# Kernel tuning notes

Hardware: AMD Instinct MI355X
Metric: run time of the kernel (lower is better)

Reference implementation:

```python
import jax, jax.numpy as jnp
import numpy as np

B, C, H, W_DIM = 32, 512, 56, 56
C_INTER = C // 2
EPS = 1e-5


def _conv1x1(x, w, b):
    # 1x1 conv == per-pixel matmul over channels. w: [out, in], b: [out]
    return jnp.einsum('bchw,oc->bohw', x, w) + b[None, :, None, None]


def setup_inputs() -> dict:
    key = jax.random.key(0)
    ks = jax.random.split(key, 5)
    s_in = 1.0 / np.sqrt(C)
    s_mid = 1.0 / np.sqrt(C_INTER)
    return {
        'x': jax.random.normal(ks[0], (B, C, H, W_DIM), dtype=jnp.float32),
        'g_w': jax.random.normal(ks[1], (C_INTER, C), dtype=jnp.float32) * s_in,
        'g_b': jnp.zeros((C_INTER,), dtype=jnp.float32),
        'theta_w': jax.random.normal(ks[2], (C_INTER, C), dtype=jnp.float32) * s_in,
        'theta_b': jnp.zeros((C_INTER,), dtype=jnp.float32),
        'phi_w': jax.random.normal(ks[3], (C_INTER, C), dtype=jnp.float32) * s_in,
        'phi_b': jnp.zeros((C_INTER,), dtype=jnp.float32),
        'W_w': jax.random.normal(ks[4], (C, C_INTER), dtype=jnp.float32) * s_mid,
        'W_b': jnp.zeros((C,), dtype=jnp.float32),
        'gamma': jnp.ones((C,), dtype=jnp.float32),
        'beta': jnp.zeros((C,), dtype=jnp.float32),
    }


def reference(x, g_w, g_b, theta_w, theta_b, phi_w, phi_b, W_w, W_b, gamma, beta):
    b, c, h, w = x.shape
    n = h * w
    g_x = _conv1x1(x, g_w, g_b).reshape(b, C_INTER, n)        # [B, C', N]
    theta_x = _conv1x1(x, theta_w, theta_b).reshape(b, C_INTER, n)
    phi_x = _conv1x1(x, phi_w, phi_b).reshape(b, C_INTER, n)
    # f = theta @ phi^T / N : small [B, C', C'] channel Gram matrix
    f_div_C = jnp.einsum('bcn,bdn->bcd', theta_x, phi_x) / n
    y = jnp.einsum('bcd,bdn->bcn', f_div_C, g_x).reshape(b, C_INTER, h, w)
    z = _conv1x1(y, W_w, W_b) + x
    # BatchNorm2d (training mode): normalize with batch stats over (B,H,W)
    mean = jnp.mean(z, axis=(0, 2, 3), keepdims=True)
    var = jnp.var(z, axis=(0, 2, 3), keepdims=True)
    z_hat = (z - mean) * jax.lax.rsqrt(var + EPS)
    return z_hat * gamma[None, :, None, None] + beta[None, :, None, None]
```

## Files before the change

kernel.cpp:

```cpp
#include <hip/hip_runtime.h>

#define Bn   32
#define Cc   512
#define CIc  256
#define Nsp  3136
#define Npad 3200
#define EPSbn 1e-5f

typedef __attribute__((ext_vector_type(8))) short v8s;
typedef __attribute__((ext_vector_type(4))) float v4f;

__device__ __forceinline__ unsigned short f2bf(float f) {
    unsigned int u = __builtin_bit_cast(unsigned int, f);
    u += 0x7fffu + ((u >> 16) & 1u);
    return (unsigned short)(u >> 16);
}

__device__ __forceinline__ float bf2f(unsigned short u) {
    unsigned int x = ((unsigned int)u) << 16;
    return __builtin_bit_cast(float, x);
}

__device__ __forceinline__ void async16(const unsigned short* g, unsigned short* l) {
    __builtin_amdgcn_global_load_lds(
        (const __attribute__((address_space(1))) unsigned int*)g,
        (__attribute__((address_space(3))) unsigned int*)l, 16, 0, 0);
}

template <int EPI>
__global__ __launch_bounds__(256)
void mfma_gemm(const unsigned short* __restrict__ A, int lda, long a_bs,
               const unsigned short* __restrict__ B, int ldb, long b_bs,
               void* __restrict__ Out, int ldo, long o_bs,
               int K, float scale,
               const float* __restrict__ biasN, long bN_bs,
               const float* __restrict__ xres,
               float* __restrict__ stats,
               const float* __restrict__ r2u1, const float* __restrict__ r2w1,
               const float* __restrict__ r2u2, const float* __restrict__ r2w2)
{
    __shared__ __align__(16) unsigned short As[128 * 32];
    __shared__ __align__(16) unsigned short Bs[128 * 32];

    const int tid  = threadIdx.x;
    const int w    = tid >> 6;
    const int lane = tid & 63;
    const int b    = blockIdx.z;
    const int m0   = blockIdx.x * 128;
    const int n0   = blockIdx.y * 128;

    const unsigned short* Ab = A + (long)b * a_bs;
    const unsigned short* Bb = B + (long)b * b_bs;

    const int ldrow = 32 * w + (lane >> 2);
    const int ldk   = (lane & 3) * 8;
    unsigned short* lA0 = &As[(2 * w + 0) * 512];
    unsigned short* lA1 = &As[(2 * w + 1) * 512];
    unsigned short* lB0 = &Bs[(2 * w + 0) * 512];
    unsigned short* lB1 = &Bs[(2 * w + 1) * 512];
    const size_t aoff0 = (size_t)(m0 + ldrow) * lda + ldk;
    const size_t aoff1 = aoff0 + (size_t)16 * lda;
    const size_t boff0 = (size_t)(n0 + ldrow) * ldb + ldk;
    const size_t boff1 = boff0 + (size_t)16 * ldb;

    const int wm = (w & 1) * 64;
    const int wn = (w >> 1) * 64;
    const int fr = lane & 15;
    const int fk = (lane >> 4) * 8;

    v4f acc[4][4] = {};

    for (int k0 = 0; k0 < K; k0 += 32) {
        __syncthreads();
        async16(Ab + aoff0 + k0, lA0);
        async16(Ab + aoff1 + k0, lA1);
        async16(Bb + boff0 + k0, lB0);
        async16(Bb + boff1 + k0, lB1);
        __syncthreads();

        v8s af[4], bf[4];
#pragma unroll
        for (int i = 0; i < 4; ++i)
            af[i] = *(const v8s*)&As[(wm + i * 16 + fr) * 32 + fk];
#pragma unroll
        for (int j = 0; j < 4; ++j)
            bf[j] = *(const v8s*)&Bs[(wn + j * 16 + fr) * 32 + fk];
#pragma unroll
        for (int i = 0; i < 4; ++i)
#pragma unroll
            for (int j = 0; j < 4; ++j)
                acc[i][j] = __builtin_amdgcn_mfma_f32_16x16x32_bf16(af[i], bf[j], acc[i][j], 0, 0, 0);
    }

    const int em = wm + ((lane >> 4) << 2);
    const int en = wn + fr;

    if constexpr (EPI == 0) {
        unsigned short* O = (unsigned short*)Out;
#pragma unroll
        for (int j = 0; j < 4; ++j) {
            const int gn = n0 + en + j * 16;
            const float bN = biasN ? biasN[bN_bs * b + gn] : 0.0f;
            unsigned short* orow = O + (long)b * o_bs + (size_t)gn * ldo + m0 + em;
#pragma unroll
            for (int i = 0; i < 4; ++i) {
                ushort4 o4;
                o4.x = f2bf(acc[i][j].x * scale + bN);
                o4.y = f2bf(acc[i][j].y * scale + bN);
                o4.z = f2bf(acc[i][j].z * scale + bN);
                o4.w = f2bf(acc[i][j].w * scale + bN);
                *(ushort4*)&orow[i * 16] = o4;
            }
        }
    } else if constexpr (EPI == 4) {
        unsigned short* O = (unsigned short*)Out;
#pragma unroll
        for (int j = 0; j < 4; ++j) {
            const int gn = n0 + en + j * 16;
            const float uu1 = r2u1[(size_t)b * Cc + gn];
            const float uu2 = r2u2[gn];
            unsigned short* orow = O + (long)b * o_bs + (size_t)gn * ldo + m0 + em;
#pragma unroll
            for (int i = 0; i < 4; ++i) {
                const int e0 = m0 + em + i * 16;
                const float4 w1v = *(const float4*)&r2w1[e0];
                const float4 w2v = *(const float4*)&r2w2[(size_t)b * Cc + e0];
                ushort4 o4;
                o4.x = f2bf(acc[i][j].x * scale + uu1 * w1v.x + uu2 * w2v.x);
                o4.y = f2bf(acc[i][j].y * scale + uu1 * w1v.y + uu2 * w2v.y);
                o4.z = f2bf(acc[i][j].z * scale + uu1 * w1v.z + uu2 * w2v.z);
                o4.w = f2bf(acc[i][j].w * scale + uu1 * w1v.w + uu2 * w2v.w);
                *(ushort4*)&orow[i * 16] = o4;
            }
        }
    } else {
        unsigned short* O = (unsigned short*)Out;
        float sj[4] = {0.f, 0.f, 0.f, 0.f}, qj[4] = {0.f, 0.f, 0.f, 0.f};
#pragma unroll
        for (int j = 0; j < 4; ++j) {
            const int gc = n0 + en + j * 16;
            const float wb = biasN[bN_bs * b + gc];
            const float* xrow = xres + (size_t)b * Cc * Nsp + (size_t)gc * Nsp;
            unsigned short* zrow = O + (long)b * o_bs + (size_t)gc * ldo;
#pragma unroll
            for (int i = 0; i < 4; ++i) {
                const int gsp = m0 + em + i * 16;
                if (gsp < Nsp) {
                    const float4 xr = *(const float4*)&xrow[gsp];
                    const float z0 = acc[i][j].x + wb + xr.x;
                    const float z1 = acc[i][j].y + wb + xr.y;
                    const float z2 = acc[i][j].z + wb + xr.z;
                    const float z3 = acc[i][j].w + wb + xr.w;
                    sj[j] += z0 + z1 + z2 + z3;
                    qj[j] += z0 * z0 + z1 * z1 + z2 * z2 + z3 * z3;
                    ushort4 o4;
                    o4.x = f2bf(z0); o4.y = f2bf(z1); o4.z = f2bf(z2); o4.w = f2bf(z3);
                    *(ushort4*)&zrow[gsp] = o4;
                }
            }
        }
        __syncthreads();
        float* red = (float*)As;
        const int cid = (lane >> 4) + ((w & 1) << 2);
#pragma unroll
        for (int j = 0; j < 4; ++j) {
            const int cc = wn + fr + j * 16;
            red[cc * 8 + cid] = sj[j];
            red[1024 + cc * 8 + cid] = qj[j];
        }
        __syncthreads();
        if (tid < 128) {
            float s = 0.f, q = 0.f;
#pragma unroll
            for (int t = 0; t < 8; ++t) { s += red[tid * 8 + t]; q += red[1024 + tid * 8 + t]; }
            atomicAdd(&stats[n0 + tid], s);
            atomicAdd(&stats[Cc + n0 + tid], q);
        }
    }
}

__global__ __launch_bounds__(256)
void cast_transpose(const float* __restrict__ x, unsigned short* __restrict__ xT,
                    unsigned short* __restrict__ x16, float* __restrict__ r)
{
    __shared__ float tile[64][65];
    const int b  = blockIdx.z;
    const int n0 = blockIdx.x * 64;
    const int c0 = blockIdx.y * 64;
    const float* xb = x + (size_t)b * Cc * Nsp;
    unsigned short* x16b = x16 + (size_t)b * Cc * Nsp;
    const int t = threadIdx.x;
    const int tr  = t >> 4;
    const int tc4 = (t & 15) * 4;
#pragma unroll
    for (int i = 0; i < 4; ++i) {
        const int c = tr + i * 16;
        const float4 v = *(const float4*)&xb[(size_t)(c0 + c) * Nsp + n0 + tc4];
        tile[tc4 + 0][c] = v.x;
        tile[tc4 + 1][c] = v.y;
        tile[tc4 + 2][c] = v.z;
        tile[tc4 + 3][c] = v.w;
        ushort4 s;
        s.x = f2bf(v.x); s.y = f2bf(v.y); s.z = f2bf(v.z); s.w = f2bf(v.w);
        *(ushort4*)&x16b[(size_t)(c0 + c) * Nsp + n0 + tc4] = s;
    }
    __syncthreads();
    if (t < 64) {
        float s = 0.f;
#pragma unroll 8
        for (int n = 0; n < 64; ++n) s += tile[n][t];
        atomicAdd(&r[(size_t)b * Cc + c0 + t], s);
    }
    unsigned short* xo = xT + (size_t)b * Nsp * Cc;
#pragma unroll
    for (int i = 0; i < 4; ++i) {
        const int n = tr + i * 16;
        ushort4 o;
        o.x = f2bf(tile[n][tc4 + 0]);
        o.y = f2bf(tile[n][tc4 + 1]);
        o.z = f2bf(tile[n][tc4 + 2]);
        o.w = f2bf(tile[n][tc4 + 3]);
        *(ushort4*)&xo[(size_t)(n0 + n) * Cc + c0 + tc4] = o;
    }
}

__global__ void cast_w(const float* __restrict__ src, unsigned short* __restrict__ dst, int n)
{
    const int i = (blockIdx.x * 256 + threadIdx.x) * 4;
    if (i < n) {
        const float4 v = *(const float4*)&src[i];
        ushort4 o;
        o.x = f2bf(v.x); o.y = f2bf(v.y); o.z = f2bf(v.z); o.w = f2bf(v.w);
        *(ushort4*)&dst[i] = o;
    }
}

__global__ void cast_wT(const float* __restrict__ src, unsigned short* __restrict__ dst)
{
    const int c = blockIdx.x;
    const int d = threadIdx.x;
    dst[(size_t)c * CIc + d] = f2bf(src[(size_t)d * Cc + c]);
}

__global__ void k_vec1(const float* __restrict__ g_w, const float* __restrict__ ph_w,
                       const float* __restrict__ W_w, const float* __restrict__ th_b,
                       const float* __restrict__ ph_b, const float* __restrict__ g_b,
                       float* __restrict__ w1, float* __restrict__ q,
                       float* __restrict__ u2, float* __restrict__ pbgb)
{
    const int t = threadIdx.x;
    float a = 0.f, bq = 0.f;
    for (int d = 0; d < CIc; ++d) {
        a  += g_w[(size_t)d * Cc + t] * ph_b[d];
        bq += ph_w[(size_t)d * Cc + t] * g_b[d];
    }
    w1[t] = a; q[t] = bq;
    float u = 0.f;
    for (int c = 0; c < CIc; ++c) u += W_w[(size_t)t * CIc + c] * th_b[c];
    u2[t] = u;
    if (t == 0) {
        float s = 0.f;
        for (int d = 0; d < CIc; ++d) s += ph_b[d] * g_b[d];
        *pbgb = s;
    }
}

__global__ void k_vecb(const unsigned short* __restrict__ S, const unsigned short* __restrict__ WT,
                       const unsigned short* __restrict__ PGt, const float* __restrict__ r,
                       const float* __restrict__ w1, const float* __restrict__ q,
                       const float* __restrict__ pbgb,
                       const float* __restrict__ th_w, const float* __restrict__ th_b,
                       const float* __restrict__ W_w, const float* __restrict__ W_b,
                       float* __restrict__ u1, float* __restrict__ w2, float* __restrict__ c0)
{
    const int b = blockIdx.x, t = threadIdx.x;
    __shared__ float sq[Cc];
    __shared__ float fgb[CIc];
    __shared__ float s_rq;
    const float invN = 1.0f / (float)Nsp;
    const float* rb = r + (size_t)b * Cc;

    float aq = 0.f;
    const unsigned short* Sr = S + (size_t)b * Cc * Cc + (size_t)t * Cc;
    for (int c2 = 0; c2 < Cc; ++c2) aq += bf2f(Sr[c2]) * q[c2];
    sq[t] = aq;

    float a1 = 0.f;
    const unsigned short* WTr = WT + (size_t)t * Cc;
    for (int c1 = 0; c1 < Cc; ++c1) a1 += bf2f(WTr[c1]) * rb[c1];
    u1[(size_t)b * Cc + t] = a1 * invN;

    float a2 = 0.f;
    const unsigned short* PGr = PGt + (size_t)t * Cc;
    for (int c2 = 0; c2 < Cc; ++c2) a2 += bf2f(PGr[c2]) * rb[c2];
    w2[(size_t)b * Cc + t] = a2 * invN + w1[t];

    if (t == 0) {
        float s = 0.f;
        for (int c2 = 0; c2 < Cc; ++c2) s += rb[c2] * q[c2];
        s_rq = s;
    }
    __syncthreads();
    if (t < CIc) {
        float ts = 0.f, tr2 = 0.f;
        const float* thr = th_w + (size_t)t * Cc;
        for (int c1 = 0; c1 < Cc; ++c1) { ts += thr[c1] * sq[c1]; tr2 += thr[c1] * rb[c1]; }
        const float pg = *pbgb;
        fgb[t] = (ts + pg * tr2 + s_rq * th_b[t]) * invN + pg * th_b[t];
    }
    __syncthreads();
    float cacc = 0.f;
    const float* Wr = W_w + (size_t)t * CIc;
    for (int d = 0; d < CIc; ++d) cacc += Wr[d] * fgb[d];
    c0[(size_t)b * Cc + t] = cacc + W_b[t];
}

__global__ void finalize_stats(const float* __restrict__ stats, float* __restrict__ mstd)
{
    const int c = threadIdx.x;
    const float inv = 1.0f / (float)((long)Bn * Nsp);
    const float mean = stats[c] * inv;
    const float var  = stats[Cc + c] * inv - mean * mean;
    mstd[c] = mean;
    mstd[Cc + c] = rsqrtf(var + EPSbn);
}

__global__ __launch_bounds__(256)
void bnorm_apply(const unsigned short* __restrict__ z, const float* __restrict__ mstd,
                 const float* __restrict__ gamma, const float* __restrict__ beta,
                 float* __restrict__ out)
{
    const int NG = Bn * Cc * (Nsp / 8);
    const int g = blockIdx.x * 256 + threadIdx.x;
    if (g >= NG) return;
    const int c = (g / (Nsp / 8)) & (Cc - 1);
    const float a1 = mstd[Cc + c] * gamma[c];
    const float a0 = beta[c] - mstd[c] * a1;
    const v8s zv = *(const v8s*)(z + (size_t)g * 8);
    float* op = out + (size_t)g * 8;
    float4 o0, o1;
    o0.x = bf2f((unsigned short)zv[0]) * a1 + a0;
    o0.y = bf2f((unsigned short)zv[1]) * a1 + a0;
    o0.z = bf2f((unsigned short)zv[2]) * a1 + a0;
    o0.w = bf2f((unsigned short)zv[3]) * a1 + a0;
    o1.x = bf2f((unsigned short)zv[4]) * a1 + a0;
    o1.y = bf2f((unsigned short)zv[5]) * a1 + a0;
    o1.z = bf2f((unsigned short)zv[6]) * a1 + a0;
    o1.w = bf2f((unsigned short)zv[7]) * a1 + a0;
    *(float4*)op = o0;
    *(float4*)(op + 4) = o1;
}

extern "C" void kernel_launch(void* const* d_in, const int* in_sizes, int n_in,
                              void* d_out, int out_size, void* d_ws, size_t ws_size,
                              hipStream_t stream)
{
    const float* x     = (const float*)d_in[0];
    const float* g_w   = (const float*)d_in[1];
    const float* g_b   = (const float*)d_in[2];
    const float* th_w  = (const float*)d_in[3];
    const float* th_b  = (const float*)d_in[4];
    const float* ph_w  = (const float*)d_in[5];
    const float* ph_b  = (const float*)d_in[6];
    const float* W_w   = (const float*)d_in[7];
    const float* W_b   = (const float*)d_in[8];
    const float* gamma = (const float*)d_in[9];
    const float* beta  = (const float*)d_in[10];
    float* out = (float*)d_out;

    unsigned short* xT   = (unsigned short*)d_ws;
    unsigned short* x16  = xT + (size_t)Bn * Nsp * Cc + 64 * Cc;
    unsigned short* S    = x16 + (size_t)Bn * Cc * Nsp;
    unsigned short* WT   = S + (size_t)Bn * Cc * Cc;
    unsigned short* PGt  = WT + (size_t)Cc * Cc;
    unsigned short* thwT = PGt + (size_t)Cc * Cc;
    unsigned short* phwT = thwT + (size_t)Cc * CIc;
    unsigned short* gwT  = phwT + (size_t)Cc * CIc;
    unsigned short* Ww16 = gwT + (size_t)Cc * CIc;
    float* r    = (float*)(Ww16 + (size_t)Cc * CIc);
    float* w1   = r + Bn * Cc;
    float* q    = w1 + Cc;
    float* u2v  = q + Cc;
    float* pbgb = u2v + Cc;
    float* u1v  = pbgb + 4;
    float* w2v  = u1v + Bn * Cc;
    float* c0   = w2v + Bn * Cc;
    float* stats = c0 + Bn * Cc;
    float* mstd  = stats + 2 * Cc;

    unsigned short* Rt    = x16;
    unsigned short* Afull = S;
    unsigned short* z16   = x16;

    hipMemsetAsync(stats, 0, 2 * Cc * sizeof(float), stream);
    hipMemsetAsync(r, 0, (size_t)Bn * Cc * sizeof(float), stream);

    const dim3 blk(256);
    const long xT_bs  = (long)Nsp * Cc;
    const long x16_bs = (long)Cc * Nsp;
    const long sq_bs  = (long)Cc * Cc;

    cast_transpose<<<dim3(49, 8, Bn), blk, 0, stream>>>(x, xT, x16, r);
    cast_w<<<dim3(128), blk, 0, stream>>>(W_w, Ww16, Cc * CIc);
    cast_wT<<<dim3(Cc), dim3(CIc), 0, stream>>>(th_w, thwT);
    cast_wT<<<dim3(Cc), dim3(CIc), 0, stream>>>(ph_w, phwT);
    cast_wT<<<dim3(Cc), dim3(CIc), 0, stream>>>(g_w, gwT);
    k_vec1<<<dim3(1), dim3(Cc), 0, stream>>>(g_w, ph_w, W_w, th_b, ph_b, g_b, w1, q, u2v, pbgb);

    mfma_gemm<0><<<dim3(4, 4, 1), blk, 0, stream>>>(
        thwT, CIc, 0, Ww16, CIc, 0, WT, Cc, 0, CIc, 1.0f,
        nullptr, 0, nullptr, nullptr, nullptr, nullptr, nullptr, nullptr);
    mfma_gemm<0><<<dim3(4, 4, 1), blk, 0, stream>>>(
        phwT, CIc, 0, gwT, CIc, 0, PGt, Cc, 0, CIc, 1.0f,
        nullptr, 0, nullptr, nullptr, nullptr, nullptr, nullptr, nullptr);
    mfma_gemm<0><<<dim3(4, 4, Bn), blk, 0, stream>>>(
        x16, Nsp, x16_bs, x16, Nsp, x16_bs, S, Cc, sq_bs, Nsp, 1.0f,
        nullptr, 0, nullptr, nullptr, nullptr, nullptr, nullptr, nullptr);
    mfma_gemm<0><<<dim3(4, 4, Bn), blk, 0, stream>>>(
        S, Cc, sq_bs, PGt, Cc, 0, Rt, Cc, sq_bs, Cc, 1.0f,
        nullptr, 0, nullptr, nullptr, nullptr, nullptr, nullptr, nullptr);
    k_vecb<<<dim3(Bn), dim3(Cc), 0, stream>>>(S, WT, PGt, r, w1, q, pbgb,
                                              th_w, th_b, W_w, W_b, u1v, w2v, c0);
    mfma_gemm<4><<<dim3(4, 4, Bn), blk, 0, stream>>>(
        Rt, Cc, sq_bs, WT, Cc, 0, Afull, Cc, sq_bs, Cc, 1.0f / (float)Nsp,
        nullptr, 0, nullptr, nullptr, u1v, w1, u2v, w2v);
    mfma_gemm<2><<<dim3(25, 4, Bn), blk, 0, stream>>>(
        xT, Cc, xT_bs, Afull, Cc, sq_bs, z16, Nsp, (long)Cc * Nsp, Cc, 1.0f,
        c0, Cc, x, stats, nullptr, nullptr, nullptr, nullptr);
    finalize_stats<<<dim3(1), dim3(Cc), 0, stream>>>(stats, mstd);
    bnorm_apply<<<dim3((Bn * Cc * (Nsp / 8) + 255) / 256), blk, 0, stream>>>(
        z16, mstd, gamma, beta, out);
}
```

Baseline: 866.1 us.

## Compute BatchNorm stats analytically from Gram matrices and fuse normalize into final GEMM

BatchNorm batch statistics are now derived algebraically from the per-batch Gram matrix S, the fused operator Afull, and per-channel row sums and sums of squares of x, using an extra small GEMM (S·Afull) and a reduction kernel. This removes the bf16 z intermediate and the separate normalize pass, because the final large GEMM can apply scale and shift directly and write fp32 output. The final GEMM also loops over all four N chunks inside one block so the xT tile is reused. In exchange it adds a 512x512 batched GEMM and more workspace, and the statistics rely on bf16-rounded operands, which may cost accuracy.

```diff
diff --git a/kernel.cpp b/kernel.cpp
--- a/kernel.cpp
+++ b/kernel.cpp
@@ -4,7 +4,6 @@
 #define Cc   512
 #define CIc  256
 #define Nsp  3136
-#define Npad 3200
 #define EPSbn 1e-5f
 
 typedef __attribute__((ext_vector_type(8))) short v8s;
@@ -27,15 +26,15 @@
         (__attribute__((address_space(3))) unsigned int*)l, 16, 0, 0);
 }
 
-template <int EPI>
+template <int EPI, int NCH>
 __global__ __launch_bounds__(256)
 void mfma_gemm(const unsigned short* __restrict__ A, int lda, long a_bs,
                const unsigned short* __restrict__ B, int ldb, long b_bs,
                void* __restrict__ Out, int ldo, long o_bs,
                int K, float scale,
                const float* __restrict__ biasN, long bN_bs,
-               const float* __restrict__ xres,
-               float* __restrict__ stats,
+               const void* __restrict__ xres,
+               const float* __restrict__ a10,
                const float* __restrict__ r2u1, const float* __restrict__ r2w1,
                const float* __restrict__ r2u2, const float* __restrict__ r2w2)
 {
@@ -47,7 +46,6 @@
     const int lane = tid & 63;
     const int b    = blockIdx.z;
     const int m0   = blockIdx.x * 128;
-    const int n0   = blockIdx.y * 128;
 
     const unsigned short* Ab = A + (long)b * a_bs;
     const unsigned short* Bb = B + (long)b * b_bs;
@@ -60,128 +58,115 @@
     unsigned short* lB1 = &Bs[(2 * w + 1) * 512];
     const size_t aoff0 = (size_t)(m0 + ldrow) * lda + ldk;
     const size_t aoff1 = aoff0 + (size_t)16 * lda;
-    const size_t boff0 = (size_t)(n0 + ldrow) * ldb + ldk;
-    const size_t boff1 = boff0 + (size_t)16 * ldb;
 
     const int wm = (w & 1) * 64;
     const int wn = (w >> 1) * 64;
     const int fr = lane & 15;
     const int fk = (lane >> 4) * 8;
 
-    v4f acc[4][4] = {};
-
-    for (int k0 = 0; k0 < K; k0 += 32) {
-        __syncthreads();
-        async16(Ab + aoff0 + k0, lA0);
-        async16(Ab + aoff1 + k0, lA1);
-        async16(Bb + boff0 + k0, lB0);
-        async16(Bb + boff1 + k0, lB1);
-        __syncthreads();
-
-        v8s af[4], bf[4];
-#pragma unroll
-        for (int i = 0; i < 4; ++i)
-            af[i] = *(const v8s*)&As[(wm + i * 16 + fr) * 32 + fk];
-#pragma unroll
-        for (int j = 0; j < 4; ++j)
-            bf[j] = *(const v8s*)&Bs[(wn + j * 16 + fr) * 32 + fk];
-#pragma unroll
-        for (int i = 0; i < 4; ++i)
-#pragma unroll
-            for (int j = 0; j < 4; ++j)
-                acc[i][j] = __builtin_amdgcn_mfma_f32_16x16x32_bf16(af[i], bf[j], acc[i][j], 0, 0, 0);
-    }
-
     const int em = wm + ((lane >> 4) << 2);
     const int en = wn + fr;
 
-    if constexpr (EPI == 0) {
-        unsigned short* O = (unsigned short*)Out;
-#pragma unroll
-        for (int j = 0; j < 4; ++j) {
-            const int gn = n0 + en + j * 16;
-            const float bN = biasN ? biasN[bN_bs * b + gn] : 0.0f;
-            unsigned short* orow = O + (long)b * o_bs + (size_t)gn * ldo + m0 + em;
-#pragma unroll
-            for (int i = 0; i < 4; ++i) {
-                ushort4 o4;
-                o4.x = f2bf(acc[i][j].x * scale + bN);
-                o4.y = f2bf(acc[i][j].y * scale + bN);
-                o4.z = f2bf(acc[i][j].z * scale + bN);
-                o4.w = f2bf(acc[i][j].w * scale + bN);
-                *(ushort4*)&orow[i * 16] = o4;
+    for (int nc = 0; nc < NCH; ++nc) {
+        const int n0 = (NCH == 1 ? (int)blockIdx.y : nc) * 128;
+        const size_t boff0 = (size_t)(n0 + ldrow) * ldb + ldk;
+        const size_t boff1 = boff0 + (size_t)16 * ldb;
+
+        v4f acc[4][4] = {};
+
+        for (int k0 = 0; k0 < K; k0 += 32) {
+            __syncthreads();
+            async16(Ab + aoff0 + k0, lA0);
+            async16(Ab + aoff1 + k0, lA1);
+            async16(Bb + boff0 + k0, lB0);
+            async16(Bb + boff1 + k0, lB1);
+            __syncthreads();
+
+            v8s af[4], bf[4];
+#pragma unroll
+            for (int i = 0; i < 4; ++i)
+                af[i] = *(const v8s*)&As[(wm + i * 16 + fr) * 32 + fk];
+#pragma unroll
+            for (int j = 0; j < 4; ++j)
+                bf[j] = *(const v8s*)&Bs[(wn + j * 16 + fr) * 32 + fk];
+#pragma unroll
+            for (int i = 0; i < 4; ++i)
+#pragma unroll
+                for (int j = 0; j < 4; ++j)
+                    acc[i][j] = __builtin_amdgcn_mfma_f32_16x16x32_bf16(af[i], bf[j], acc[i][j], 0, 0, 0);
+        }
+
+        if constexpr (EPI == 0) {
+            unsigned short* O = (unsigned short*)Out;
+#pragma unroll
+            for (int j = 0; j < 4; ++j) {
+                const int gn = n0 + en + j * 16;
+                const float bN = biasN ? biasN[bN_bs * b + gn] : 0.0f;
+                unsigned short* orow = O + (long)b * o_bs + (size_t)gn * ldo + m0 + em;
+#pragma unroll
+                for (int i = 0; i < 4; ++i) {
+                    ushort4 o4;
+                    o4.x = f2bf(acc[i][j].x * scale + bN);
+                    o4.y = f2bf(acc[i][j].y * scale + bN);
+                    o4.z = f2bf(acc[i][j].z * scale + bN);
+                    o4.w = f2bf(acc[i][j].w * scale + bN);
+                    *(ushort4*)&orow[i * 16] = o4;
+                }
             }
-        }
-    } else if constexpr (EPI == 4) {
-        unsigned short* O = (unsigned short*)Out;
-#pragma unroll
-        for (int j = 0; j < 4; ++j) {
-            const int gn = n0 + en + j * 16;
-            const float uu1 = r2u1[(size_t)b * Cc + gn];
-            const float uu2 = r2u2[gn];
-            unsigned short* orow = O + (long)b * o_bs + (size_t)gn * ldo + m0 + em;
-#pragma unroll
-            for (int i = 0; i < 4; ++i) {
-                const int e0 = m0 + em + i * 16;
-                const float4 w1v = *(const float4*)&r2w1[e0];
-                const float4 w2v = *(const float4*)&r2w2[(size_t)b * Cc + e0];
-                ushort4 o4;
-                o4.x = f2bf(acc[i][j].x * scale + uu1 * w1v.x + uu2 * w2v.x);
-                o4.y = f2bf(acc[i][j].y * scale + uu1 * w1v.y + uu2 * w2v.y);
-                o4.z = f2bf(acc[i][j].z * scale + uu1 * w1v.z + uu2 * w2v.z);
-                o4.w = f2bf(acc[i][j].w * scale + uu1 * w1v.w + uu2 * w2v.w);
-                *(ushort4*)&orow[i * 16] = o4;
+        } else if constexpr (EPI == 4) {
+            unsigned short* O = (unsigned short*)Out;
+#pragma unroll
+            for (int j = 0; j < 4; ++j) {
+                const int gn = n0 + en + j * 16;
+                const float uu1 = r2u1[(size_t)b * Cc + gn];
+                const float uu2 = r2u2[gn];
+                unsigned short* orow = O + (long)b * o_bs + (size_t)gn * ldo + m0 + em;
+#pragma unroll
+                for (int i = 0; i < 4; ++i) {
+                    const int e0 = m0 + em + i * 16;
+                    const float4 w1v = *(const float4*)&r2w1[e0];
+                    const float4 w2v = *(const float4*)&r2w2[(size_t)b * Cc + e0];
+                    ushort4 o4;
+                    o4.x = f2bf(acc[i][j].x * scale + uu1 * w1v.x + uu2 * w2v.x);
+                    o4.y = f2bf(acc[i][j].y * scale + uu1 * w1v.y + uu2 * w2v.y);
+                    o4.z = f2bf(acc[i][j].z * scale + uu1 * w1v.z + uu2 * w2v.z);
+                    o4.w = f2bf(acc[i][j].w * scale + uu1 * w1v.w + uu2 * w2v.w);
+                    *(ushort4*)&orow[i * 16] = o4;
+                }
             }
-        }
-    } else {
-        unsigned short* O = (unsigned short*)Out;
-        float sj[4] = {0.f, 0.f, 0.f, 0.f}, qj[4] = {0.f, 0.f, 0.f, 0.f};
-#pragma unroll
-        for (int j = 0; j < 4; ++j) {
-            const int gc = n0 + en + j * 16;
-            const float wb = biasN[bN_bs * b + gc];
-            const float* xrow = xres + (size_t)b * Cc * Nsp + (size_t)gc * Nsp;
-            unsigned short* zrow = O + (long)b * o_bs + (size_t)gc * ldo;
-#pragma unroll
-            for (int i = 0; i < 4; ++i) {
-                const int gsp = m0 + em + i * 16;
-                if (gsp < Nsp) {
-                    const float4 xr = *(const float4*)&xrow[gsp];
-                    const float z0 = acc[i][j].x + wb + xr.x;
-                    const float z1 = acc[i][j].y + wb + xr.y;
-                    const float z2 = acc[i][j].z + wb + xr.z;
-                    const float z3 = acc[i][j].w + wb + xr.w;
-                    sj[j] += z0 + z1 + z2 + z3;
-                    qj[j] += z0 * z0 + z1 * z1 + z2 * z2 + z3 * z3;
-                    ushort4 o4;
-                    o4.x = f2bf(z0); o4.y = f2bf(z1); o4.z = f2bf(z2); o4.w = f2bf(z3);
-                    *(ushort4*)&zrow[gsp] = o4;
+        } else {
+            float* O = (float*)Out;
+            const unsigned short* xr16 = (const unsigned short*)xres;
+#pragma unroll
+            for (int j = 0; j < 4; ++j) {
+                const int gc = n0 + en + j * 16;
+                const float a1 = a10[gc];
+                const float a0 = a10[Cc + gc];
+                const float cc0 = biasN[bN_bs * b + gc];
+                const unsigned short* xrow = xr16 + (size_t)b * Cc * Nsp + (size_t)gc * Nsp;
+                float* orow = O + (long)b * o_bs + (size_t)gc * (size_t)ldo;
+#pragma unroll
+                for (int i = 0; i < 4; ++i) {
+                    const int gsp = m0 + em + i * 16;
+                    if (gsp < Nsp) {
+                        const ushort4 xr = *(const ushort4*)&xrow[gsp];
+                        float4 o;
+                        o.x = (acc[i][j].x + cc0 + bf2f(xr.x)) * a1 + a0;
+                        o.y = (acc[i][j].y + cc0 + bf2f(xr.y)) * a1 + a0;
+                        o.z = (acc[i][j].z + cc0 + bf2f(xr.z)) * a1 + a0;
+                        o.w = (acc[i][j].w + cc0 + bf2f(xr.w)) * a1 + a0;
+                        *(float4*)&orow[gsp] = o;
+                    }
                 }
             }
         }
-        __syncthreads();
-        float* red = (float*)As;
-        const int cid = (lane >> 4) + ((w & 1) << 2);
-#pragma unroll
-        for (int j = 0; j < 4; ++j) {
-            const int cc = wn + fr + j * 16;
-            red[cc * 8 + cid] = sj[j];
-            red[1024 + cc * 8 + cid] = qj[j];
-        }
-        __syncthreads();
-        if (tid < 128) {
-            float s = 0.f, q = 0.f;
-#pragma unroll
-            for (int t = 0; t < 8; ++t) { s += red[tid * 8 + t]; q += red[1024 + tid * 8 + t]; }
-            atomicAdd(&stats[n0 + tid], s);
-            atomicAdd(&stats[Cc + n0 + tid], q);
-        }
     }
 }
 
 __global__ __launch_bounds__(256)
 void cast_transpose(const float* __restrict__ x, unsigned short* __restrict__ xT,
-                    unsigned short* __restrict__ x16, float* __restrict__ r)
+                    unsigned short* __restrict__ x16, float* __restrict__ r,
+                    float* __restrict__ p)
 {
     __shared__ float tile[64][65];
     const int b  = blockIdx.z;
@@ -192,6 +177,7 @@
     const int t = threadIdx.x;
     const int tr  = t >> 4;
     const int tc4 = (t & 15) * 4;
+    float rs[4], ps[4];
 #pragma unroll
     for (int i = 0; i < 4; ++i) {
         const int c = tr + i * 16;
@@ -203,14 +189,26 @@
         ushort4 s;
         s.x = f2bf(v.x); s.y = f2bf(v.y); s.z = f2bf(v.z); s.w = f2bf(v.w);
         *(ushort4*)&x16b[(size_t)(c0 + c) * Nsp + n0 + tc4] = s;
+        const float b0 = bf2f(s.x), b1 = bf2f(s.y), b2 = bf2f(s.z), b3 = bf2f(s.w);
+        rs[i] = b0 + b1 + b2 + b3;
+        ps[i] = b0 * b0 + b1 * b1 + b2 * b2 + b3 * b3;
+    }
+#pragma unroll
+    for (int i = 0; i < 4; ++i) {
+#pragma unroll
+        for (int off = 8; off; off >>= 1) {
+            rs[i] += __shfl_down(rs[i], off, 16);
+            ps[i] += __shfl_down(ps[i], off, 16);
+        }
+    }
+    if ((t & 15) == 0) {
+#pragma unroll
+        for (int i = 0; i < 4; ++i) {
+            atomicAdd(&r[(size_t)b * Cc + c0 + tr + i * 16], rs[i]);
+            atomicAdd(&p[(size_t)b * Cc + c0 + tr + i * 16], ps[i]);
+        }
     }
     __syncthreads();
-    if (t < 64) {
-        float s = 0.f;
-#pragma unroll 8
-        for (int n = 0; n < 64; ++n) s += tile[n][t];
-        atomicAdd(&r[(size_t)b * Cc + c0 + t], s);
-    }
     unsigned short* xo = xT + (size_t)b * Nsp * Cc;
 #pragma unroll
     for (int i = 0; i < 4; ++i) {
@@ -315,40 +313,54 @@
     c0[(size_t)b * Cc + t] = cacc + W_b[t];
 }
 
-__global__ void finalize_stats(const float* __restrict__ stats, float* __restrict__ mstd)
+__global__ __launch_bounds__(256)
+void k_stats(const unsigned short* __restrict__ Afull, const unsigned short* __restrict__ AS,
+             const float* __restrict__ r, const float* __restrict__ p,
+             const float* __restrict__ c0, float* __restrict__ stats)
+{
+    const int b = blockIdx.x;
+    const int f = blockIdx.y * 4 + (threadIdx.x >> 6);
+    const int lane = threadIdx.x & 63;
+    const size_t row = ((size_t)b * Cc + f) * Cc;
+    const v8s av = *(const v8s*)(Afull + row + lane * 8);
+    const v8s sv = *(const v8s*)(AS + row + lane * 8);
+    const float* rb = r + (size_t)b * Cc + lane * 8;
+    float d1 = 0.f, ar = 0.f;
+#pragma unroll
+    for (int k = 0; k < 8; ++k) {
+        const float a = bf2f((unsigned short)av[k]);
+        d1 += a * bf2f((unsigned short)sv[k]);
+        ar += a * rb[k];
+    }
+#pragma unroll
+    for (int off = 32; off; off >>= 1) {
+        d1 += __shfl_down(d1, off);
+        ar += __shfl_down(ar, off);
+    }
+    if (lane == 0) {
+        const float cc   = c0[(size_t)b * Cc + f];
+        const float rf   = r[(size_t)b * Cc + f];
+        const float pf   = p[(size_t)b * Cc + f];
+        const float asff = bf2f(AS[row + f]);
+        const float sum = ar + rf + (float)Nsp * cc;
+        const float ss  = d1 + 2.f * cc * ar + (float)Nsp * cc * cc
+                        + 2.f * asff + 2.f * cc * rf + pf;
+        atomicAdd(&stats[f], sum);
+        atomicAdd(&stats[Cc + f], ss);
+    }
+}
+
+__global__ void finalize_stats(const float* __restrict__ stats,
+                               const float* __restrict__ gamma, const float* __restrict__ beta,
+                               float* __restrict__ a10)
 {
     const int c = threadIdx.x;
     const float inv = 1.0f / (float)((long)Bn * Nsp);
     const float mean = stats[c] * inv;
     const float var  = stats[Cc + c] * inv - mean * mean;
-    mstd[c] = mean;
-    mstd[Cc + c] = rsqrtf(var + EPSbn);
-}
-
-__global__ __launch_bounds__(256)
-void bnorm_apply(const unsigned short* __restrict__ z, const float* __restrict__ mstd,
-                 const float* __restrict__ gamma, const float* __restrict__ beta,
-                 float* __restrict__ out)
-{
-    const int NG = Bn * Cc * (Nsp / 8);
-    const int g = blockIdx.x * 256 + threadIdx.x;
-    if (g >= NG) return;
-    const int c = (g / (Nsp / 8)) & (Cc - 1);
-    const float a1 = mstd[Cc + c] * gamma[c];
-    const float a0 = beta[c] - mstd[c] * a1;
-    const v8s zv = *(const v8s*)(z + (size_t)g * 8);
-    float* op = out + (size_t)g * 8;
-    float4 o0, o1;
-    o0.x = bf2f((unsigned short)zv[0]) * a1 + a0;
-    o0.y = bf2f((unsigned short)zv[1]) * a1 + a0;
-    o0.z = bf2f((unsigned short)zv[2]) * a1 + a0;
-    o0.w = bf2f((unsigned short)zv[3]) * a1 + a0;
-    o1.x = bf2f((unsigned short)zv[4]) * a1 + a0;
-    o1.y = bf2f((unsigned short)zv[5]) * a1 + a0;
-    o1.z = bf2f((unsigned short)zv[6]) * a1 + a0;
-    o1.w = bf2f((unsigned short)zv[7]) * a1 + a0;
-    *(float4*)op = o0;
-    *(float4*)(op + 4) = o1;
+    const float a1 = rsqrtf(var + EPSbn) * gamma[c];
+    a10[c] = a1;
+    a10[Cc + c] = beta[c] - mean * a1;
 }
 
 extern "C" void kernel_launch(void* const* d_in, const int* in_sizes, int n_in,
@@ -371,14 +383,17 @@
     unsigned short* xT   = (unsigned short*)d_ws;
     unsigned short* x16  = xT + (size_t)Bn * Nsp * Cc + 64 * Cc;
     unsigned short* S    = x16 + (size_t)Bn * Cc * Nsp;
-    unsigned short* WT   = S + (size_t)Bn * Cc * Cc;
+    unsigned short* R1   = S + (size_t)Bn * Cc * Cc;
+    unsigned short* R2   = R1 + (size_t)Bn * Cc * Cc;
+    unsigned short* WT   = R2 + (size_t)Bn * Cc * Cc;
     unsigned short* PGt  = WT + (size_t)Cc * Cc;
     unsigned short* thwT = PGt + (size_t)Cc * Cc;
     unsigned short* phwT = thwT + (size_t)Cc * CIc;
     unsigned short* gwT  = phwT + (size_t)Cc * CIc;
     unsigned short* Ww16 = gwT + (size_t)Cc * CIc;
     float* r    = (float*)(Ww16 + (size_t)Cc * CIc);
-    float* w1   = r + Bn * Cc;
+    float* p    = r + Bn * Cc;
+    float* w1   = p + Bn * Cc;
     float* q    = w1 + Cc;
     float* u2v  = q + Cc;
     float* pbgb = u2v + Cc;
@@ -386,48 +401,50 @@
     float* w2v  = u1v + Bn * Cc;
     float* c0   = w2v + Bn * Cc;
     float* stats = c0 + Bn * Cc;
-    float* mstd  = stats + 2 * Cc;
-
-    unsigned short* Rt    = x16;
-    unsigned short* Afull = S;
-    unsigned short* z16   = x16;
+    float* a10   = stats + 2 * Cc;
+
+    unsigned short* Rt    = R1;
+    unsigned short* Afull = R2;
+    unsigned short* AS    = R1;
 
     hipMemsetAsync(stats, 0, 2 * Cc * sizeof(float), stream);
-    hipMemsetAsync(r, 0, (size_t)Bn * Cc * sizeof(float), stream);
+    hipMemsetAsync(r, 0, 2 * (size_t)Bn * Cc * sizeof(float), stream);
 
     const dim3 blk(256);
     const long xT_bs  = (long)Nsp * Cc;
     const long x16_bs = (long)Cc * Nsp;
     const long sq_bs  = (long)Cc * Cc;
 
-    cast_transpose<<<dim3(49, 8, Bn), blk, 0, stream>>>(x, xT, x16, r);
+    cast_transpose<<<dim3(49, 8, Bn), blk, 0, stream>>>(x, xT, x16, r, p);
     cast_w<<<dim3(128), blk, 0, stream>>>(W_w, Ww16, Cc * CIc);
     cast_wT<<<dim3(Cc), dim3(CIc), 0, stream>>>(th_w, thwT);
     cast_wT<<<dim3(Cc), dim3(CIc), 0, stream>>>(ph_w, phwT);
     cast_wT<<<dim3(Cc), dim3(CIc), 0, stream>>>(g_w, gwT);
     k_vec1<<<dim3(1), dim3(Cc), 0, stream>>>(g_w, ph_w, W_w, th_b, ph_b, g_b, w1, q, u2v, pbgb);
 
-    mfma_gemm<0><<<dim3(4, 4, 1), blk, 0, stream>>>(
+    mfma_gemm<0, 1><<<dim3(4, 4, 1), blk, 0, stream>>>(
         thwT, CIc, 0, Ww16, CIc, 0, WT, Cc, 0, CIc, 1.0f,
         nullptr, 0, nullptr, nullptr, nullptr, nullptr, nullptr, nullptr);
-    mfma_gemm<0><<<dim3(4, 4, 1), blk, 0, stream>>>(
+    mfma_gemm<0, 1><<<dim3(4, 4, 1), blk, 0, stream>>>(
         phwT, CIc, 0, gwT, CIc, 0, PGt, Cc, 0, CIc, 1.0f,
         nullptr, 0, nullptr, nullptr, nullptr, nullptr, nullptr, nullptr);
-    mfma_gemm<0><<<dim3(4, 4, Bn), blk, 0, stream>>>(
+    mfma_gemm<0, 1><<<dim3(4, 4, Bn), blk, 0, stream>>>(
         x16, Nsp, x16_bs, x16, Nsp, x16_bs, S, Cc, sq_bs, Nsp, 1.0f,
         nullptr, 0, nullptr, nullptr, nullptr, nullptr, nullptr, nullptr);
-    mfma_gemm<0><<<dim3(4, 4, Bn), blk, 0, stream>>>(
+    mfma_gemm<0, 1><<<dim3(4, 4, Bn), blk, 0, stream>>>(
         S, Cc, sq_bs, PGt, Cc, 0, Rt, Cc, sq_bs, Cc, 1.0f,
         nullptr, 0, nullptr, nullptr, nullptr, nullptr, nullptr, nullptr);
     k_vecb<<<dim3(Bn), dim3(Cc), 0, stream>>>(S, WT, PGt, r, w1, q, pbgb,
                                               th_w, th_b, W_w, W_b, u1v, w2v, c0);
-    mfma_gemm<4><<<dim3(4, 4, Bn), blk, 0, stream>>>(
+    mfma_gemm<4, 1><<<dim3(4, 4, Bn), blk, 0, stream>>>(
         Rt, Cc, sq_bs, WT, Cc, 0, Afull, Cc, sq_bs, Cc, 1.0f / (float)Nsp,
         nullptr, 0, nullptr, nullptr, u1v, w1, u2v, w2v);
-    mfma_gemm<2><<<dim3(25, 4, Bn), blk, 0, stream>>>(
-        xT, Cc, xT_bs, Afull, Cc, sq_bs, z16, Nsp, (long)Cc * Nsp, Cc, 1.0f,
-        c0, Cc, x, stats, nullptr, nullptr, nullptr, nullptr);
-    finalize_stats<<<dim3(1), dim3(Cc), 0, stream>>>(stats, mstd);
-    bnorm_apply<<<dim3((Bn * Cc * (Nsp / 8) + 255) / 256), blk, 0, stream>>>(
-        z16, mstd, gamma, beta, out);
-}
+    mfma_gemm<0, 1><<<dim3(4, 4, Bn), blk, 0, stream>>>(
+        S, Cc, sq_bs, Afull, Cc, sq_bs, AS, Cc, sq_bs, Cc, 1.0f,
+        nullptr, 0, nullptr, nullptr, nullptr, nullptr, nullptr, nullptr);
+    k_stats<<<dim3(Bn, 128), blk, 0, stream>>>(Afull, AS, r, p, c0, stats);
+    finalize_stats<<<dim3(1), dim3(Cc), 0, stream>>>(stats, gamma, beta, a10);
+    mfma_gemm<5, 4><<<dim3(25, 1, Bn), blk, 0, stream>>>(
+        xT, Cc, xT_bs, Afull, Cc, sq_bs, out, Nsp, (long)Cc * Nsp, Cc, 1.0f,
+        c0, Cc, x16, a10, nullptr, nullptr, nullptr, nullptr);
+}
```

After: 887.2 us. +2.4%, slower.
